# Optimization experiments

Measured on AMD Instinct MI355X. Metric: run time of the kernel, lower is better.

## Reference

```python
import jax, jax.numpy as jnp
import numpy as np

H = 64  # LSTM hidden size per direction


def _lstm_dir(x, Wih, Whh, b, reverse):
    # x: [B,T,I]; Wih: [4H,I]; Whh: [4H,H]; b: [4H] (b_ih + b_hh combined)
    if reverse:
        x = x[:, ::-1]
    xg = jnp.einsum('bti,gi->btg', x, Wih) + b  # precompute input gates [B,T,4H]
    B = x.shape[0]
    WhhT = Whh.T  # [H,4H]

    def step(carry, xt_g):
        h, c = carry
        g = xt_g + h @ WhhT  # [B,4H]
        i, f, gg, o = jnp.split(g, 4, axis=-1)  # PyTorch gate order i,f,g,o
        c = jax.nn.sigmoid(f) * c + jax.nn.sigmoid(i) * jnp.tanh(gg)
        h = jax.nn.sigmoid(o) * jnp.tanh(c)
        return (h, c), h

    h0 = jnp.zeros((B, H), x.dtype)
    _, hs = jax.lax.scan(step, (h0, h0), jnp.swapaxes(xg, 0, 1))
    hs = jnp.swapaxes(hs, 0, 1)  # [B,T,H]
    if reverse:
        hs = hs[:, ::-1]
    return hs


def _bilstm(x, wih_f, whh_f, b_f, wih_b, whh_b, b_b):
    fwd = _lstm_dir(x, wih_f, whh_f, b_f, False)
    bwd = _lstm_dir(x, wih_b, whh_b, b_b, True)
    return jnp.concatenate([fwd, bwd], axis=-1)  # [B,T,2H]


def setup_inputs() -> dict:
    key = jax.random.key(0)
    ks = jax.random.split(key, 16)
    B, IN = 8192, 20

    def w(k, shape, fan_in):
        return jax.random.normal(k, shape, jnp.float32) * (1.0 / np.sqrt(fan_in))

    inp = {
        'x': jax.random.normal(ks[0], (B, IN), jnp.float32),
        'fc1_w': w(ks[1], (50, IN), IN),
        'fc1_b': jnp.zeros((50,), jnp.float32),
        # rnn1: input_size=1, bidirectional
        'r1_wih_f': w(ks[2], (4 * H, 1), 1),
        'r1_whh_f': w(ks[3], (4 * H, H), H),
        'r1_b_f': jnp.zeros((4 * H,), jnp.float32),
        'r1_wih_b': w(ks[4], (4 * H, 1), 1),
        'r1_whh_b': w(ks[5], (4 * H, H), H),
        'r1_b_b': jnp.zeros((4 * H,), jnp.float32),
        # rnn2: input_size=2H=128, bidirectional
        'r2_wih_f': w(ks[6], (4 * H, 2 * H), 2 * H),
        'r2_whh_f': w(ks[7], (4 * H, H), H),
        'r2_b_f': jnp.zeros((4 * H,), jnp.float32),
        'r2_wih_b': w(ks[8], (4 * H, 2 * H), 2 * H),
        'r2_whh_b': w(ks[9], (4 * H, H), H),
        'r2_b_b': jnp.zeros((4 * H,), jnp.float32),
        'fc2_w': w(ks[10], (1, 2 * H), 2 * H),
        'fc2_b': jnp.zeros((1,), jnp.float32),
    }
    return inp


def reference(x, fc1_w, fc1_b,
              r1_wih_f, r1_whh_f, r1_b_f, r1_wih_b, r1_whh_b, r1_b_b,
              r2_wih_f, r2_whh_f, r2_b_f, r2_wih_b, r2_whh_b, r2_b_b,
              fc2_w, fc2_b):
    h = x @ fc1_w.T + fc1_b            # [B,50]
    h = h[..., None]                   # [B,50,1]
    h = _bilstm(h, r1_wih_f, r1_whh_f, r1_b_f, r1_wih_b, r1_whh_b, r1_b_b)  # [B,50,128]
    h = jnp.repeat(h, 2, axis=1)       # nearest upsample x2 along time -> [B,100,128]
    h = _bilstm(h, r2_wih_f, r2_whh_f, r2_b_f, r2_wih_b, r2_whh_b, r2_b_b)  # [B,100,128]
    out = jnp.tanh(jnp.einsum('btf,of->bto', h, fc2_w) + fc2_b)  # [B,100,1]
    return out
```

## Files before the change

kernel.cpp:

```cpp
#include <hip/hip_runtime.h>
#include <cmath>

#define H1    64
#define T1    50
#define T2    100
#define BATCH 8192
#define NB2   256
#define NTILE 512

typedef __attribute__((ext_vector_type(8))) short s16x8;
typedef __attribute__((ext_vector_type(4))) float f32x4;

#define MFMA16(a,b,c) __builtin_amdgcn_mfma_f32_16x16x32_bf16(a,b,c,0,0,0)

#define S_SIG  (-1.4426950408889634f)
#define S_TANH ( 2.8853900817779268f)

#define OFF_FC1T  ((size_t)0)
#define OFF_XF    ((size_t)1638400)
#define OFF_WA1   ((size_t)(1638400 + 104857600))
#define OFF_WA2HH (OFF_WA1 + 65536)
#define OFF_WA2IH (OFF_WA2HH + 65536)
#define OFF_PART  (OFF_WA2IH + 131072)

__device__ __forceinline__ float rcp_(float x) { return __builtin_amdgcn_rcpf(x); }
__device__ __forceinline__ float exp2_(float x) {
#if __has_builtin(__builtin_amdgcn_exp2f)
    return __builtin_amdgcn_exp2f(x);
#else
    return exp2f(x);
#endif
}
__device__ __forceinline__ float sigp_(float e)  { return rcp_(1.f + exp2_(e)); }
__device__ __forceinline__ float tanhp_(float e) { return 1.f - 2.f * rcp_(1.f + exp2_(e)); }
__device__ __forceinline__ float tanhc_(float c) { return tanhp_(S_TANH * c); }
__device__ __forceinline__ float tanh_(float x)  { return tanhc_(x); }

__device__ __forceinline__ unsigned short bf16_rne(float x) {
    unsigned int u = __float_as_uint(x);
    u += 0x7fffu + ((u >> 16) & 1u);
    return (unsigned short)(u >> 16);
}
__device__ __forceinline__ float bf16f(unsigned short h) {
    return __uint_as_float(((unsigned int)h) << 16);
}

__global__ __launch_bounds__(256) void k_prep(
    const float* __restrict__ whh1f, const float* __restrict__ whh1b,
    const float* __restrict__ whh2f, const float* __restrict__ whh2b,
    const float* __restrict__ wih2f, const float* __restrict__ wih2b,
    unsigned short* __restrict__ WA1, unsigned short* __restrict__ WA2HH,
    unsigned short* __restrict__ WA2IH)
{
    int i = blockIdx.x * 256 + threadIdx.x;
    if (i < 8192) {
        int a   = i >> 12;
        int r   = i & 4095;
        int dir = r >> 11, rem = r & 2047;
        int mt  = rem >> 7, rem2 = rem & 127;
        int kk  = rem2 >> 6, l = rem2 & 63;
        const float* s_ = a ? (dir ? whh2b : whh2f) : (dir ? whh1b : whh1f);
        unsigned short* d_ = a ? WA2HH : WA1;
        int gate = mt * 16 + (l & 15);
        float sc = ((gate >> 6) == 2) ? S_TANH : S_SIG;
        int k0   = kk * 32 + (l >> 4) * 8;
        const float* p = s_ + gate * 64 + k0;
        unsigned short* q = d_ + (size_t)r * 8;
#pragma unroll
        for (int j = 0; j < 8; ++j) q[j] = bf16_rne(p[j] * sc);
    } else {
        int r   = i - 8192;
        int dir = r >> 12, rem = r & 4095;
        int mt  = rem >> 8, rem2 = rem & 255;
        int kk  = rem2 >> 6, l = rem2 & 63;
        const float* s_ = dir ? wih2b : wih2f;
        int gate = mt * 16 + (l & 15);
        float sc = ((gate >> 6) == 2) ? S_TANH : S_SIG;
        int k0   = kk * 32 + (l >> 4) * 8;
        const float* p = s_ + gate * 128 + k0;
        unsigned short* q = WA2IH + (size_t)r * 8;
#pragma unroll
        for (int j = 0; j < 8; ++j) q[j] = bf16_rne(p[j] * sc);
    }
}

__global__ __launch_bounds__(256) void k_fc1(const float* __restrict__ x,
                                             const float* __restrict__ w,
                                             const float* __restrict__ b,
                                             float* __restrict__ fc1T) {
    __shared__ float wls[1000];
    __shared__ float bls[50];
    int tid = threadIdx.x;
    for (int i = tid; i < 1000; i += 256) wls[i] = w[i];
    if (tid < 50) bls[tid] = b[tid];
    __syncthreads();
    int bidx = blockIdx.x * 256 + tid;
    float xv[20];
#pragma unroll
    for (int i = 0; i < 20; ++i) xv[i] = x[bidx * 20 + i];
    for (int t = 0; t < T1; ++t) {
        float s = bls[t];
#pragma unroll
        for (int i = 0; i < 20; ++i) s += xv[i] * wls[t * 20 + i];
        fc1T[t * BATCH + bidx] = s;
    }
}

__global__ __launch_bounds__(512, 4) void k_lstm1(
    const float* __restrict__ wih1f, const float* __restrict__ b1f,
    const float* __restrict__ wih1b, const float* __restrict__ b1b,
    const unsigned short* __restrict__ WA1,
    const float* __restrict__ fc1T,
    unsigned short* __restrict__ XF)
{
    __shared__ float x1s[T1][32];
    __shared__ unsigned short Htf[2][2][2][2][64][8];
    int tid  = threadIdx.x;
    int lane = tid & 63;
    int w    = __builtin_amdgcn_readfirstlane(tid >> 6);
    int wh   = w & 3, wsh = w >> 2;
    int quad = lane >> 4, col = lane & 15;
    int dir  = blockIdx.y, bblk = blockIdx.x;

    for (int i = tid; i < T1 * 32; i += 512) {
        int t = i >> 5, s = i & 31;
        x1s[t][s] = fc1T[t * BATCH + bblk * 32 + s];
    }
    const float* wih = dir ? wih1b : wih1f;
    const float* bia = dir ? b1b : b1f;
    f32x4 wvv[4], bvv[4];
#pragma unroll
    for (int g = 0; g < 4; ++g) {
        float sc = (g == 2) ? S_TANH : S_SIG;
#pragma unroll
        for (int r = 0; r < 4; ++r) {
            int gate = g * 64 + wh * 16 + quad * 4 + r;
            wvv[g][r] = wih[gate] * sc;
            bvv[g][r] = bia[gate] * sc;
        }
    }
    s16x8 whhA[4][2];
#pragma unroll
    for (int g = 0; g < 4; ++g)
#pragma unroll
        for (int kk = 0; kk < 2; ++kk)
            whhA[g][kk] = *(const s16x8*)(WA1 +
                ((size_t)((dir * 16 + (g * 4 + wh)) * 2 + kk) * 64 + lane) * 8);

    float c[4];
#pragma unroll
    for (int r = 0; r < 4; ++r) c[r] = 0.f;

    int lq  = 2 * (wh & 1) + (quad >> 1);
    int lp  = lq * 16 + col;
    int jo  = (quad & 1) * 4;
    int kkw = wh >> 1;
    int kk1 = dir * 2 + (wh >> 1);
    int gtile = bblk * 2 + wsh;
    __syncthreads();
    int buf = 0;
    for (int step = 0; step < T1; ++step) {
        int t = dir ? (T1 - 1 - step) : step;
        float xt = x1s[t][wsh * 16 + col];
        f32x4 acc[4];
#pragma unroll
        for (int g = 0; g < 4; ++g)
#pragma unroll
            for (int r = 0; r < 4; ++r)
                acc[g][r] = bvv[g][r] + wvv[g][r] * xt;
        if (step) {
#pragma unroll
            for (int hf = 0; hf < 2; ++hf) {
                s16x8 hb0 = *(const s16x8*)&Htf[buf][hf][0][wsh][lane][0];
                s16x8 hb1 = *(const s16x8*)&Htf[buf][hf][1][wsh][lane][0];
#pragma unroll
                for (int g = 0; g < 4; ++g) {
                    acc[g] = MFMA16(whhA[g][0], hb0, acc[g]);
                    acc[g] = MFMA16(whhA[g][1], hb1, acc[g]);
                }
            }
        }
        int nbuf = buf ^ 1;
        unsigned short hh[4], hl[4];
#pragma unroll
        for (int r = 0; r < 4; ++r) {
            float cc = sigp_(acc[1][r]) * c[r] + sigp_(acc[0][r]) * tanhp_(acc[2][r]);
            c[r] = cc;
            float h = sigp_(acc[3][r]) * tanhc_(cc);
            hh[r] = bf16_rne(h);
            hl[r] = bf16_rne(h - bf16f(hh[r]));
        }
        uint2 vhi, vlo;
        vhi.x = (unsigned)hh[0] | ((unsigned)hh[1] << 16);
        vhi.y = (unsigned)hh[2] | ((unsigned)hh[3] << 16);
        vlo.x = (unsigned)hl[0] | ((unsigned)hl[1] << 16);
        vlo.y = (unsigned)hl[2] | ((unsigned)hl[3] << 16);
        *(uint2*)&Htf[nbuf][0][kkw][wsh][lp][jo] = vhi;
        *(uint2*)&Htf[nbuf][1][kkw][wsh][lp][jo] = vlo;
        *(uint2*)(XF + ((((size_t)t * 4 + kk1) * NTILE + gtile) * 64 + lp) * 8 + jo) = vhi;
        __syncthreads();
        buf = nbuf;
    }
}

__global__ __launch_bounds__(512, 4) void k_lstm2(
    const float* __restrict__ b2f, const float* __restrict__ b2b,
    const float* __restrict__ fc2w,
    const unsigned short* __restrict__ WA2HH,
    const unsigned short* __restrict__ WA2IH,
    const unsigned short* __restrict__ XF,
    float* __restrict__ part)
{
    __shared__ unsigned short wAl[16][4][64][8];
    __shared__ unsigned short Htf[2][2][2][64][8];
    __shared__ f32x4 biasl[16][4];
    __shared__ float partb[2][4][16];
    int tid  = threadIdx.x;
    int lane = tid & 63;
    int w    = __builtin_amdgcn_readfirstlane(tid >> 6);
    int wh   = w & 3, wsh = w >> 2;
    int quad = lane >> 4, col = lane & 15;
    int dir  = blockIdx.y, bblk = blockIdx.x;
    int gtile = bblk * 2 + wsh;

    {
        const uint4* src = (const uint4*)(WA2IH + (size_t)dir * 32768);
        uint4* dst = (uint4*)&wAl[0][0][0][0];
        for (int i = tid; i < 4096; i += 512) dst[i] = src[i];
    }
    const float* bia = dir ? b2b : b2f;
    if (tid < 64) {
        int mt = tid >> 2, q = tid & 3;
        float sc = ((mt >> 2) == 2) ? S_TANH : S_SIG;
        f32x4 v;
#pragma unroll
        for (int r = 0; r < 4; ++r) v[r] = bia[mt * 16 + q * 4 + r] * sc;
        biasl[mt][q] = v;
    }
    float f2v[4];
#pragma unroll
    for (int r = 0; r < 4; ++r)
        f2v[r] = fc2w[dir * 64 + wh * 16 + quad * 4 + r];

    s16x8 whhA[4][2];
#pragma unroll
    for (int g = 0; g < 4; ++g)
#pragma unroll
        for (int kk = 0; kk < 2; ++kk)
            whhA[g][kk] = *(const s16x8*)(WA2HH +
                ((size_t)((dir * 16 + (g * 4 + wh)) * 2 + kk) * 64 + lane) * 8);

    float c[4];
#pragma unroll
    for (int r = 0; r < 4; ++r) c[r] = 0.f;

    int lq  = 2 * (wh & 1) + (quad >> 1);
    int lp  = lq * 16 + col;
    int jo  = (quad & 1) * 4;
    int kkw = wh >> 1;
    f32x4 xacc[4];
    __syncthreads();

    for (int step = 0; step < T2; ++step) {
        int t2 = dir ? (T2 - 1 - step) : step;
        if ((step & 1) == 0) {
            int tp = t2 >> 1;
#pragma unroll
            for (int g = 0; g < 4; ++g) xacc[g] = biasl[g * 4 + wh][quad];
#pragma unroll
            for (int kk = 0; kk < 4; ++kk) {
                s16x8 xbk = *(const s16x8*)(XF +
                    (((size_t)(tp * 4 + kk) * NTILE + gtile) * 64 + lane) * 8);
#pragma unroll
                for (int g = 0; g < 4; ++g) {
                    s16x8 wa = *(const s16x8*)&wAl[g * 4 + wh][kk][lane][0];
                    xacc[g] = MFMA16(wa, xbk, xacc[g]);
                }
            }
        }
        f32x4 acc[4];
#pragma unroll
        for (int g = 0; g < 4; ++g) acc[g] = xacc[g];
        if (step) {
#pragma unroll
            for (int hf = 0; hf < 2; ++hf) {
                s16x8 hb0 = *(const s16x8*)&Htf[hf][0][wsh][lane][0];
                s16x8 hb1 = *(const s16x8*)&Htf[hf][1][wsh][lane][0];
#pragma unroll
                for (int g = 0; g < 4; ++g) {
                    acc[g] = MFMA16(whhA[g][0], hb0, acc[g]);
                    acc[g] = MFMA16(whhA[g][1], hb1, acc[g]);
                }
            }
        }
        unsigned short hh[4], hl[4];
        float pacc = 0.f;
#pragma unroll
        for (int r = 0; r < 4; ++r) {
            float cc = sigp_(acc[1][r]) * c[r] + sigp_(acc[0][r]) * tanhp_(acc[2][r]);
            c[r] = cc;
            float h = sigp_(acc[3][r]) * tanhc_(cc);
            pacc += f2v[r] * h;
            hh[r] = bf16_rne(h);
            hl[r] = bf16_rne(h - bf16f(hh[r]));
        }
        pacc += __shfl_xor(pacc, 16);
        pacc += __shfl_xor(pacc, 32);
        uint2 vhi, vlo;
        vhi.x = (unsigned)hh[0] | ((unsigned)hh[1] << 16);
        vhi.y = (unsigned)hh[2] | ((unsigned)hh[3] << 16);
        vlo.x = (unsigned)hl[0] | ((unsigned)hl[1] << 16);
        vlo.y = (unsigned)hl[2] | ((unsigned)hl[3] << 16);
        __syncthreads();
        *(uint2*)&Htf[0][kkw][wsh][lp][jo] = vhi;
        *(uint2*)&Htf[1][kkw][wsh][lp][jo] = vlo;
        if (lane < 16) partb[wsh][wh][lane] = pacc;
        __syncthreads();
        if (tid < 32) {
            int sw = tid >> 4, sc_ = tid & 15;
            float p = partb[sw][0][sc_] + partb[sw][1][sc_] +
                      partb[sw][2][sc_] + partb[sw][3][sc_];
            part[((size_t)(dir * T2 + t2)) * BATCH + bblk * 32 + tid] = p;
        }
    }
}

__global__ __launch_bounds__(256) void k_fc2(const float* __restrict__ part,
                                             const float* __restrict__ fc2b,
                                             float* __restrict__ out) {
    int u = blockIdx.x * 256 + threadIdx.x;
    if (u >= BATCH * T2) return;
    int b = u / T2, t = u - b * T2;
    float p = part[(size_t)t * BATCH + b] + part[((size_t)T2 + t) * BATCH + b] + fc2b[0];
    out[u] = tanh_(p);
}

extern "C" void kernel_launch(void* const* d_in, const int* in_sizes, int n_in,
                              void* d_out, int out_size, void* d_ws, size_t ws_size,
                              hipStream_t stream) {
    const float* x      = (const float*)d_in[0];
    const float* fc1w   = (const float*)d_in[1];
    const float* fc1b   = (const float*)d_in[2];
    const float* r1wihf = (const float*)d_in[3];
    const float* r1whhf = (const float*)d_in[4];
    const float* r1bf   = (const float*)d_in[5];
    const float* r1wihb = (const float*)d_in[6];
    const float* r1whhb = (const float*)d_in[7];
    const float* r1bb   = (const float*)d_in[8];
    const float* r2wihf = (const float*)d_in[9];
    const float* r2whhf = (const float*)d_in[10];
    const float* r2bf   = (const float*)d_in[11];
    const float* r2wihb = (const float*)d_in[12];
    const float* r2whhb = (const float*)d_in[13];
    const float* r2bb   = (const float*)d_in[14];
    const float* fc2w   = (const float*)d_in[15];
    const float* fc2b   = (const float*)d_in[16];
    char* ws   = (char*)d_ws;
    float* out = (float*)d_out;

    float*          fc1T  = (float*)(ws + OFF_FC1T);
    unsigned short* XF    = (unsigned short*)(ws + OFF_XF);
    unsigned short* WA1   = (unsigned short*)(ws + OFF_WA1);
    unsigned short* WA2HH = (unsigned short*)(ws + OFF_WA2HH);
    unsigned short* WA2IH = (unsigned short*)(ws + OFF_WA2IH);
    float*          partp = (float*)(ws + OFF_PART);

    k_prep<<<64, 256, 0, stream>>>(r1whhf, r1whhb, r2whhf, r2whhb, r2wihf, r2wihb,
                                   WA1, WA2HH, WA2IH);
    k_fc1<<<BATCH / 256, 256, 0, stream>>>(x, fc1w, fc1b, fc1T);
    dim3 g1(NB2, 2);
    k_lstm1<<<g1, 512, 0, stream>>>(r1wihf, r1bf, r1wihb, r1bb, WA1, fc1T, XF);
    k_lstm2<<<g1, 512, 0, stream>>>(r2bf, r2bb, fc2w, WA2HH, WA2IH, XF, partp);
    k_fc2<<<(BATCH * T2 + 255) / 256, 256, 0, stream>>>(partp, fc2b, out);
}
```

Before: 389.0 us.

## Restructure lstm2 step loop: double-buffer h, prefetch XF, atomic partials, fuse prep kernels

Merges the weight-prep and fc1 kernels into one launch, which also zeroes the partial buffer and precomputes scaled layer-2 biases. In the layer-2 recurrence, the hidden state is double-buffered in LDS so each step needs one barrier instead of two. The next timestep's XF operands are prefetched into registers, and h's high bf16 half is taken by truncation rather than round-to-nearest. Per-wave fc2 partial sums now go to global memory with atomicAdd instead of an LDS reduction, which adds atomic traffic and makes the summation order nondeterministic.

```diff
diff --git a/kernel.cpp b/kernel.cpp
--- a/kernel.cpp
+++ b/kernel.cpp
@@ -22,6 +22,7 @@
 #define OFF_WA2HH (OFF_WA1 + 65536)
 #define OFF_WA2IH (OFF_WA2HH + 65536)
 #define OFF_PART  (OFF_WA2IH + 131072)
+#define OFF_BS    (OFF_PART + 6553600)
 
 __device__ __forceinline__ float rcp_(float x) { return __builtin_amdgcn_rcpf(x); }
 __device__ __forceinline__ float exp2_(float x) {
@@ -45,64 +46,76 @@
     return __uint_as_float(((unsigned int)h) << 16);
 }
 
-__global__ __launch_bounds__(256) void k_prep(
+__global__ __launch_bounds__(256) void k_pre(
     const float* __restrict__ whh1f, const float* __restrict__ whh1b,
     const float* __restrict__ whh2f, const float* __restrict__ whh2b,
     const float* __restrict__ wih2f, const float* __restrict__ wih2b,
+    const float* __restrict__ b2f,   const float* __restrict__ b2b,
+    const float* __restrict__ x, const float* __restrict__ fc1w,
+    const float* __restrict__ fc1b,
     unsigned short* __restrict__ WA1, unsigned short* __restrict__ WA2HH,
-    unsigned short* __restrict__ WA2IH)
+    unsigned short* __restrict__ WA2IH, float* __restrict__ fc1T,
+    float* __restrict__ part, float* __restrict__ BS)
 {
-    int i = blockIdx.x * 256 + threadIdx.x;
-    if (i < 8192) {
-        int a   = i >> 12;
-        int r   = i & 4095;
-        int dir = r >> 11, rem = r & 2047;
-        int mt  = rem >> 7, rem2 = rem & 127;
-        int kk  = rem2 >> 6, l = rem2 & 63;
-        const float* s_ = a ? (dir ? whh2b : whh2f) : (dir ? whh1b : whh1f);
-        unsigned short* d_ = a ? WA2HH : WA1;
-        int gate = mt * 16 + (l & 15);
-        float sc = ((gate >> 6) == 2) ? S_TANH : S_SIG;
-        int k0   = kk * 32 + (l >> 4) * 8;
-        const float* p = s_ + gate * 64 + k0;
-        unsigned short* q = d_ + (size_t)r * 8;
-#pragma unroll
-        for (int j = 0; j < 8; ++j) q[j] = bf16_rne(p[j] * sc);
-    } else {
-        int r   = i - 8192;
-        int dir = r >> 12, rem = r & 4095;
-        int mt  = rem >> 8, rem2 = rem & 255;
-        int kk  = rem2 >> 6, l = rem2 & 63;
-        const float* s_ = dir ? wih2b : wih2f;
-        int gate = mt * 16 + (l & 15);
-        float sc = ((gate >> 6) == 2) ? S_TANH : S_SIG;
-        int k0   = kk * 32 + (l >> 4) * 8;
-        const float* p = s_ + gate * 128 + k0;
-        unsigned short* q = WA2IH + (size_t)r * 8;
-#pragma unroll
-        for (int j = 0; j < 8; ++j) q[j] = bf16_rne(p[j] * sc);
-    }
-}
-
-__global__ __launch_bounds__(256) void k_fc1(const float* __restrict__ x,
-                                             const float* __restrict__ w,
-                                             const float* __restrict__ b,
-                                             float* __restrict__ fc1T) {
     __shared__ float wls[1000];
     __shared__ float bls[50];
     int tid = threadIdx.x;
-    for (int i = tid; i < 1000; i += 256) wls[i] = w[i];
-    if (tid < 50) bls[tid] = b[tid];
-    __syncthreads();
-    int bidx = blockIdx.x * 256 + tid;
-    float xv[20];
-#pragma unroll
-    for (int i = 0; i < 20; ++i) xv[i] = x[bidx * 20 + i];
-    for (int t = 0; t < T1; ++t) {
-        float s = bls[t];
-#pragma unroll
-        for (int i = 0; i < 20; ++i) s += xv[i] * wls[t * 20 + i];
-        fc1T[t * BATCH + bidx] = s;
+    int blk = blockIdx.x;
+    if (blk < 64) {
+        int i = blk * 256 + tid;
+        if (i < 8192) {
+            int a   = i >> 12;
+            int r   = i & 4095;
+            int dir = r >> 11, rem = r & 2047;
+            int mt  = rem >> 7, rem2 = rem & 127;
+            int kk  = rem2 >> 6, l = rem2 & 63;
+            const float* s_ = a ? (dir ? whh2b : whh2f) : (dir ? whh1b : whh1f);
+            unsigned short* d_ = a ? WA2HH : WA1;
+            int gate = mt * 16 + (l & 15);
+            float sc = ((gate >> 6) == 2) ? S_TANH : S_SIG;
+            int k0   = kk * 32 + (l >> 4) * 8;
+            const float* p = s_ + gate * 64 + k0;
+            unsigned short* q = d_ + (size_t)r * 8;
+#pragma unroll
+            for (int j = 0; j < 8; ++j) q[j] = bf16_rne(p[j] * sc);
+        } else {
+            int r   = i - 8192;
+            int dir = r >> 12, rem = r & 4095;
+            int mt  = rem >> 8, rem2 = rem & 255;
+            int kk  = rem2 >> 6, l = rem2 & 63;
+            const float* s_ = dir ? wih2b : wih2f;
+            int gate = mt * 16 + (l & 15);
+            float sc = ((gate >> 6) == 2) ? S_TANH : S_SIG;
+            int k0   = kk * 32 + (l >> 4) * 8;
+            const float* p = s_ + gate * 128 + k0;
+            unsigned short* q = WA2IH + (size_t)r * 8;
+#pragma unroll
+            for (int j = 0; j < 8; ++j) q[j] = bf16_rne(p[j] * sc);
+        }
+    } else if (blk < 96) {
+        for (int i = tid; i < 1000; i += 256) wls[i] = fc1w[i];
+        if (tid < 50) bls[tid] = fc1b[tid];
+        __syncthreads();
+        int bidx = (blk - 64) * 256 + tid;
+        float xv[20];
+#pragma unroll
+        for (int i = 0; i < 20; ++i) xv[i] = x[bidx * 20 + i];
+        for (int t = 0; t < T1; ++t) {
+            float s = bls[t];
+#pragma unroll
+            for (int i = 0; i < 20; ++i) s += xv[i] * wls[t * 20 + i];
+            fc1T[t * BATCH + bidx] = s;
+        }
+    } else if (blk < 352) {
+        const int n = 2 * T2 * BATCH;
+        for (int i = (blk - 96) * 256 + tid; i < n; i += 256 * 256) part[i] = 0.f;
+    } else {
+        for (int i = tid; i < 512; i += 256) {
+            int d = i >> 8, m = i & 255;
+            const float* bb = d ? b2b : b2f;
+            float sc = ((m >> 6) == 2) ? S_TANH : S_SIG;
+            BS[i] = bb[m] * sc;
+        }
     }
 }
 
@@ -204,7 +217,7 @@
 }
 
 __global__ __launch_bounds__(512, 4) void k_lstm2(
-    const float* __restrict__ b2f, const float* __restrict__ b2b,
+    const float* __restrict__ BS,
     const float* __restrict__ fc2w,
     const unsigned short* __restrict__ WA2HH,
     const unsigned short* __restrict__ WA2IH,
@@ -212,9 +225,7 @@
     float* __restrict__ part)
 {
     __shared__ unsigned short wAl[16][4][64][8];
-    __shared__ unsigned short Htf[2][2][2][64][8];
-    __shared__ f32x4 biasl[16][4];
-    __shared__ float partb[2][4][16];
+    __shared__ unsigned short Htf[2][2][2][2][64][8];
     int tid  = threadIdx.x;
     int lane = tid & 63;
     int w    = __builtin_amdgcn_readfirstlane(tid >> 6);
@@ -228,15 +239,6 @@
         uint4* dst = (uint4*)&wAl[0][0][0][0];
         for (int i = tid; i < 4096; i += 512) dst[i] = src[i];
     }
-    const float* bia = dir ? b2b : b2f;
-    if (tid < 64) {
-        int mt = tid >> 2, q = tid & 3;
-        float sc = ((mt >> 2) == 2) ? S_TANH : S_SIG;
-        f32x4 v;
-#pragma unroll
-        for (int r = 0; r < 4; ++r) v[r] = bia[mt * 16 + q * 4 + r] * sc;
-        biasl[mt][q] = v;
-    }
     float f2v[4];
 #pragma unroll
     for (int r = 0; r < 4; ++r)
@@ -249,6 +251,8 @@
         for (int kk = 0; kk < 2; ++kk)
             whhA[g][kk] = *(const s16x8*)(WA2HH +
                 ((size_t)((dir * 16 + (g * 4 + wh)) * 2 + kk) * 64 + lane) * 8);
+
+    const float4* bsp = (const float4*)(BS + dir * 256 + wh * 16 + quad * 4);
 
     float c[4];
 #pragma unroll
@@ -258,42 +262,61 @@
     int lp  = lq * 16 + col;
     int jo  = (quad & 1) * 4;
     int kkw = wh >> 1;
+
+    s16x8 xbC[4], xbN[4];
+    {
+        int tp0 = dir ? (T1 - 1) : 0;
+#pragma unroll
+        for (int kk = 0; kk < 4; ++kk)
+            xbC[kk] = *(const s16x8*)(XF +
+                (((size_t)(tp0 * 4 + kk) * NTILE + gtile) * 64 + lane) * 8);
+    }
     f32x4 xacc[4];
     __syncthreads();
+    int buf = 0;
 
     for (int step = 0; step < T2; ++step) {
         int t2 = dir ? (T2 - 1 - step) : step;
         if ((step & 1) == 0) {
-            int tp = t2 >> 1;
-#pragma unroll
-            for (int g = 0; g < 4; ++g) xacc[g] = biasl[g * 4 + wh][quad];
-#pragma unroll
-            for (int kk = 0; kk < 4; ++kk) {
-                s16x8 xbk = *(const s16x8*)(XF +
-                    (((size_t)(tp * 4 + kk) * NTILE + gtile) * 64 + lane) * 8);
-#pragma unroll
-                for (int g = 0; g < 4; ++g) {
+#pragma unroll
+            for (int g = 0; g < 4; ++g) {
+                float4 bv4 = bsp[g * 16];
+                f32x4 a; a[0] = bv4.x; a[1] = bv4.y; a[2] = bv4.z; a[3] = bv4.w;
+#pragma unroll
+                for (int kk = 0; kk < 4; ++kk) {
                     s16x8 wa = *(const s16x8*)&wAl[g * 4 + wh][kk][lane][0];
-                    xacc[g] = MFMA16(wa, xbk, xacc[g]);
+                    a = MFMA16(wa, xbC[kk], a);
                 }
+                xacc[g] = a;
             }
+            int tp  = t2 >> 1;
+            int tpn = dir ? (tp > 0 ? tp - 1 : 0) : (tp < T1 - 1 ? tp + 1 : T1 - 1);
+#pragma unroll
+            for (int kk = 0; kk < 4; ++kk)
+                xbN[kk] = *(const s16x8*)(XF +
+                    (((size_t)(tpn * 4 + kk) * NTILE + gtile) * 64 + lane) * 8);
         }
         f32x4 acc[4];
-#pragma unroll
-        for (int g = 0; g < 4; ++g) acc[g] = xacc[g];
         if (step) {
-#pragma unroll
-            for (int hf = 0; hf < 2; ++hf) {
-                s16x8 hb0 = *(const s16x8*)&Htf[hf][0][wsh][lane][0];
-                s16x8 hb1 = *(const s16x8*)&Htf[hf][1][wsh][lane][0];
-#pragma unroll
-                for (int g = 0; g < 4; ++g) {
-                    acc[g] = MFMA16(whhA[g][0], hb0, acc[g]);
-                    acc[g] = MFMA16(whhA[g][1], hb1, acc[g]);
-                }
+            s16x8 hb00 = *(const s16x8*)&Htf[buf][0][0][wsh][lane][0];
+            s16x8 hb01 = *(const s16x8*)&Htf[buf][0][1][wsh][lane][0];
+            s16x8 hb10 = *(const s16x8*)&Htf[buf][1][0][wsh][lane][0];
+            s16x8 hb11 = *(const s16x8*)&Htf[buf][1][1][wsh][lane][0];
+#pragma unroll
+            for (int g = 0; g < 4; ++g) {
+                f32x4 a = MFMA16(whhA[g][0], hb00, xacc[g]);
+                a = MFMA16(whhA[g][1], hb01, a);
+                a = MFMA16(whhA[g][0], hb10, a);
+                a = MFMA16(whhA[g][1], hb11, a);
+                acc[g] = a;
             }
-        }
-        unsigned short hh[4], hl[4];
+        } else {
+#pragma unroll
+            for (int g = 0; g < 4; ++g) acc[g] = xacc[g];
+        }
+        int nbuf = buf ^ 1;
+        unsigned int uhi[4];
+        unsigned short hl[4];
         float pacc = 0.f;
 #pragma unroll
         for (int r = 0; r < 4; ++r) {
@@ -301,26 +324,26 @@
             c[r] = cc;
             float h = sigp_(acc[3][r]) * tanhc_(cc);
             pacc += f2v[r] * h;
-            hh[r] = bf16_rne(h);
-            hl[r] = bf16_rne(h - bf16f(hh[r]));
-        }
+            unsigned int u = __float_as_uint(h);
+            uhi[r] = u & 0xFFFF0000u;
+            hl[r]  = bf16_rne(h - __uint_as_float(uhi[r]));
+        }
+        uint2 vhi, vlo;
+        vhi.x = (uhi[0] >> 16) | uhi[1];
+        vhi.y = (uhi[2] >> 16) | uhi[3];
+        vlo.x = (unsigned)hl[0] | ((unsigned)hl[1] << 16);
+        vlo.y = (unsigned)hl[2] | ((unsigned)hl[3] << 16);
+        *(uint2*)&Htf[nbuf][0][kkw][wsh][lp][jo] = vhi;
+        *(uint2*)&Htf[nbuf][1][kkw][wsh][lp][jo] = vlo;
         pacc += __shfl_xor(pacc, 16);
         pacc += __shfl_xor(pacc, 32);
-        uint2 vhi, vlo;
-        vhi.x = (unsigned)hh[0] | ((unsigned)hh[1] << 16);
-        vhi.y = (unsigned)hh[2] | ((unsigned)hh[3] << 16);
-        vlo.x = (unsigned)hl[0] | ((unsigned)hl[1] << 16);
-        vlo.y = (unsigned)hl[2] | ((unsigned)hl[3] << 16);
+        if (lane < 16)
+            atomicAdd(&part[((size_t)(dir * T2 + t2)) * BATCH + bblk * 32 + wsh * 16 + lane], pacc);
         __syncthreads();
-        *(uint2*)&Htf[0][kkw][wsh][lp][jo] = vhi;
-        *(uint2*)&Htf[1][kkw][wsh][lp][jo] = vlo;
-        if (lane < 16) partb[wsh][wh][lane] = pacc;
-        __syncthreads();
-        if (tid < 32) {
-            int sw = tid >> 4, sc_ = tid & 15;
-            float p = partb[sw][0][sc_] + partb[sw][1][sc_] +
-                      partb[sw][2][sc_] + partb[sw][3][sc_];
-            part[((size_t)(dir * T2 + t2)) * BATCH + bblk * 32 + tid] = p;
+        buf = nbuf;
+        if (step & 1) {
+#pragma unroll
+            for (int kk = 0; kk < 4; ++kk) xbC[kk] = xbN[kk];
         }
     }
 }
@@ -364,12 +387,13 @@
     unsigned short* WA2HH = (unsigned short*)(ws + OFF_WA2HH);
     unsigned short* WA2IH = (unsigned short*)(ws + OFF_WA2IH);
     float*          partp = (float*)(ws + OFF_PART);
-
-    k_prep<<<64, 256, 0, stream>>>(r1whhf, r1whhb, r2whhf, r2whhb, r2wihf, r2wihb,
-                                   WA1, WA2HH, WA2IH);
-    k_fc1<<<BATCH / 256, 256, 0, stream>>>(x, fc1w, fc1b, fc1T);
+    float*          BS    = (float*)(ws + OFF_BS);
+
+    k_pre<<<353, 256, 0, stream>>>(r1whhf, r1whhb, r2whhf, r2whhb, r2wihf, r2wihb,
+                                   r2bf, r2bb, x, fc1w, fc1b,
+                                   WA1, WA2HH, WA2IH, fc1T, partp, BS);
     dim3 g1(NB2, 2);
     k_lstm1<<<g1, 512, 0, stream>>>(r1wihf, r1bf, r1wihb, r1bb, WA1, fc1T, XF);
-    k_lstm2<<<g1, 512, 0, stream>>>(r2bf, r2bb, fc2w, WA2HH, WA2IH, XF, partp);
+    k_lstm2<<<g1, 512, 0, stream>>>(BS, fc2w, WA2HH, WA2IH, XF, partp);
     k_fc2<<<(BATCH * T2 + 255) / 256, 256, 0, stream>>>(partp, fc2b, out);
 }
```

Measured after the change: 383.2 us. No clear change (-1.5%).
